# Kernel tuning notes

Hardware: AMD Instinct MI355X
Metric: run time of the kernel (lower is better)

The kernel has to match this reference:

```python
import jax, jax.numpy as jnp
import numpy as np

N_HEAD = 16

def setup_inputs() -> dict:
    key = jax.random.key(0)
    ks = jax.random.split(key, 9)
    B, T, C = 4, 2048, 1024
    s = 1.0 / np.sqrt(C)
    return {
        "x":  jax.random.normal(ks[0], (B, T, C), jnp.float32),
        "Wq": jax.random.normal(ks[1], (C, C), jnp.float32) * s,
        "bq": jax.random.normal(ks[2], (C,), jnp.float32) * 0.02,
        "Wk": jax.random.normal(ks[3], (C, C), jnp.float32) * s,
        "bk": jax.random.normal(ks[4], (C,), jnp.float32) * 0.02,
        "Wv": jax.random.normal(ks[5], (C, C), jnp.float32) * s,
        "bv": jax.random.normal(ks[6], (C,), jnp.float32) * 0.02,
        "Wp": jax.random.normal(ks[7], (C, C), jnp.float32) * s,
        "bp": jax.random.normal(ks[8], (C,), jnp.float32) * 0.02,
    }

def reference(x, Wq, bq, Wk, bk, Wv, bv, Wp, bp):
    B, T, C = x.shape
    H, D = N_HEAD, C // N_HEAD
    # torch nn.Linear: y = x @ W^T + b
    q = (x @ Wq.T + bq).reshape(B, T, H, D).transpose(0, 2, 1, 3)  # [B,H,T,D]
    k = (x @ Wk.T + bk).reshape(B, T, H, D).transpose(0, 2, 1, 3)
    v = (x @ Wv.T + bv).reshape(B, T, H, D).transpose(0, 2, 1, 3)
    # full TxT causal attention (non-flash path)
    att = jnp.einsum('bhtd,bhsd->bhts', q, k) * (1.0 / np.sqrt(D))  # [B,H,T,T]
    causal = jnp.tril(jnp.ones((T, T), dtype=bool))
    att = jnp.where(causal[None, None], att, -jnp.inf)
    att = jax.nn.softmax(att, axis=-1)
    y = jnp.einsum('bhts,bhsd->bhtd', att, v)  # [B,H,T,D]
    y = y.transpose(0, 2, 1, 3).reshape(B, T, C)
    return y @ Wp.T + bp
```

## Files before the change

### kernel.cpp

```cpp
#include <hip/hip_runtime.h>

typedef __bf16 bf16_t;
typedef __bf16 bf16x8 __attribute__((ext_vector_type(8)));
typedef float f32x4 __attribute__((ext_vector_type(4)));
typedef unsigned short ushort_t;

#define T_SEQ 2048
#define C_DIM 1024
#define NH    16
#define HD    64

__device__ __forceinline__ ushort_t f2bf(float f) {
    unsigned u = __builtin_bit_cast(unsigned, f);
    u += 0x7FFFu + ((u >> 16) & 1u);
    return (ushort_t)(u >> 16);
}

#define X4  2097152
#define W4  262144
__global__ __launch_bounds__(256)
void cvt_all_kernel(const float* __restrict__ x,  const float* __restrict__ Wq,
                    const float* __restrict__ Wk, const float* __restrict__ Wv,
                    ushort_t* __restrict__ xb,  ushort_t* __restrict__ Wqb,
                    ushort_t* __restrict__ Wkb, ushort_t* __restrict__ Wvb) {
    int i = blockIdx.x * 256 + threadIdx.x;
    const float* src; ushort_t* dst; int off;
    if (i < X4)                { src = x;  dst = xb;  off = i; }
    else if (i < X4 + W4)      { src = Wq; dst = Wqb; off = i - X4; }
    else if (i < X4 + 2 * W4)  { src = Wk; dst = Wkb; off = i - X4 - W4; }
    else                       { src = Wv; dst = Wvb; off = i - X4 - 2 * W4; }
    float4 f = ((const float4*)src)[off];
    ushort4 u;
    u.x = f2bf(f.x); u.y = f2bf(f.y); u.z = f2bf(f.z); u.w = f2bf(f.w);
    ((ushort4*)dst)[off] = u;
}

template<bool AF32, bool BF32>
__device__ __forceinline__ void gemm_core_128(const void* __restrict__ Araw,
                                              const void* __restrict__ Braw,
                                              f32x4 (&acc)[4][4]) {
    __shared__ alignas(16) ushort_t As[128 * 72];
    __shared__ alignas(16) ushort_t Ws[128 * 72];
    const int tid  = threadIdx.x;
    const int lane = tid & 63;
    const int wv   = tid >> 6;
    const int wm   = wv >> 1, wn = wv & 1;
    const int quad = lane >> 4, ln = lane & 15;
    const int m0 = blockIdx.x * 128, n0 = blockIdx.y * 128;

    f32x4 z4 = {0.f, 0.f, 0.f, 0.f};
#pragma unroll
    for (int i = 0; i < 4; i++)
#pragma unroll
        for (int j = 0; j < 4; j++) acc[i][j] = z4;

    for (int kt = 0; kt < 1024; kt += 64) {
        if (AF32) {
            const float* A = (const float*)Araw;
#pragma unroll
            for (int p = 0; p < 8; ++p) {
                int cid = p * 256 + tid;
                int row = cid >> 4, c4 = (cid & 15) * 4;
                float4 f = *(const float4*)(A + (size_t)(m0 + row) * 1024 + kt + c4);
                ushort4 u;
                u.x = f2bf(f.x); u.y = f2bf(f.y); u.z = f2bf(f.z); u.w = f2bf(f.w);
                *(ushort4*)&As[row * 72 + c4] = u;
            }
        } else {
            const bf16_t* A = (const bf16_t*)Araw;
#pragma unroll
            for (int p = 0; p < 4; ++p) {
                int cid = p * 256 + tid;
                int row = cid >> 3, c8 = (cid & 7) * 8;
                *(uint4*)&As[row * 72 + c8] =
                    *(const uint4*)(A + (size_t)(m0 + row) * 1024 + kt + c8);
            }
        }
        if (BF32) {
            const float* Bm = (const float*)Braw;
#pragma unroll
            for (int p = 0; p < 8; ++p) {
                int cid = p * 256 + tid;
                int row = cid >> 4, c4 = (cid & 15) * 4;
                float4 f = *(const float4*)(Bm + (size_t)(n0 + row) * 1024 + kt + c4);
                ushort4 u;
                u.x = f2bf(f.x); u.y = f2bf(f.y); u.z = f2bf(f.z); u.w = f2bf(f.w);
                *(ushort4*)&Ws[row * 72 + c4] = u;
            }
        } else {
            const bf16_t* Bm = (const bf16_t*)Braw;
#pragma unroll
            for (int p = 0; p < 4; ++p) {
                int cid = p * 256 + tid;
                int row = cid >> 3, c8 = (cid & 7) * 8;
                *(uint4*)&Ws[row * 72 + c8] =
                    *(const uint4*)(Bm + (size_t)(n0 + row) * 1024 + kt + c8);
            }
        }
        __syncthreads();
#pragma unroll
        for (int ks = 0; ks < 2; ++ks) {
            bf16x8 af[4], bfr[4];
#pragma unroll
            for (int i = 0; i < 4; i++)
                af[i] = *(const bf16x8*)&As[(wm * 64 + i * 16 + ln) * 72 + ks * 32 + quad * 8];
#pragma unroll
            for (int j = 0; j < 4; j++)
                bfr[j] = *(const bf16x8*)&Ws[(wn * 64 + j * 16 + ln) * 72 + ks * 32 + quad * 8];
#pragma unroll
            for (int i = 0; i < 4; i++)
#pragma unroll
                for (int j = 0; j < 4; j++)
                    acc[i][j] = __builtin_amdgcn_mfma_f32_16x16x32_bf16(af[i], bfr[j],
                                                                        acc[i][j], 0, 0, 0);
        }
        __syncthreads();
    }
}

__global__ __launch_bounds__(256, 2)
void qkv_gemm_kernel(const bf16_t* __restrict__ xb,
                     const bf16_t* __restrict__ Wqb, const float* __restrict__ bq,
                     const bf16_t* __restrict__ Wkb, const float* __restrict__ bk,
                     const bf16_t* __restrict__ Wvb, const float* __restrict__ bv,
                     ushort_t* __restrict__ Qo, ushort_t* __restrict__ Ko,
                     ushort_t* __restrict__ Vo) {
    const int z = blockIdx.z;
    const bf16_t* W   = (z == 0) ? Wqb : (z == 1) ? Wkb : Wvb;
    const float* bias = (z == 0) ? bq : (z == 1) ? bk : bv;
    ushort_t* outp    = (z == 0) ? Qo : (z == 1) ? Ko : Vo;
    const float fs    = (z == 0) ? 0.18033688011112042f : 1.0f;

    f32x4 acc[4][4];
    gemm_core_128<false, false>(xb, W, acc);

    const int tid  = threadIdx.x;
    const int lane = tid & 63;
    const int wv2  = tid >> 6;
    const int wm   = wv2 >> 1, wn = wv2 & 1;
    const int quad = lane >> 4, ln = lane & 15;
    const int mbase = blockIdx.x * 128 + wm * 64;
    const int nbase = blockIdx.y * 128 + wn * 64;

#pragma unroll
    for (int j = 0; j < 4; j++) {
        int n = nbase + j * 16 + ln;
        float bj = bias[n];
        int h = n >> 6, d = n & 63;
#pragma unroll
        for (int i = 0; i < 4; i++) {
            int mr = mbase + i * 16 + quad * 4;
            int b = mr >> 11;
            int t = mr & 2047;
            if (z < 2) {
                ushort_t* op = outp + ((size_t)(b * NH + h) * T_SEQ + t) * HD + d;
#pragma unroll
                for (int r = 0; r < 4; r++)
                    op[(size_t)r * HD] = f2bf((acc[i][j][r] + bj) * fs);
            } else {
                ushort4 us;
                us.x = f2bf(acc[i][j][0] + bj);
                us.y = f2bf(acc[i][j][1] + bj);
                us.z = f2bf(acc[i][j][2] + bj);
                us.w = f2bf(acc[i][j][3] + bj);
                *(ushort4*)(outp + ((size_t)(b * NH + h) * HD + d) * T_SEQ + t) = us;
            }
        }
    }
}

__device__ __forceinline__ void attn_tile(const ushort_t* __restrict__ Ks,
                                          const ushort_t* __restrict__ Vts,
                                          bf16_t* __restrict__ PsW,
                                          bf16x8 aq0, bf16x8 aq1, bf16x8 ones,
                                          f32x4 (&o)[4], f32x4& l4,
                                          bool diag, int wv, int quad, int ln) {
    f32x4 s4[4];
#pragma unroll
    for (int n16 = 0; n16 < 4; n16++) {
        f32x4 zz = {0.f, 0.f, 0.f, 0.f};
        bf16x8 bk0 = *(const bf16x8*)&Ks[(n16 * 16 + ln) * 72 + quad * 8];
        zz = __builtin_amdgcn_mfma_f32_16x16x32_bf16(aq0, bk0, zz, 0, 0, 0);
        bf16x8 bk1 = *(const bf16x8*)&Ks[(n16 * 16 + ln) * 72 + 32 + quad * 8];
        zz = __builtin_amdgcn_mfma_f32_16x16x32_bf16(aq1, bk1, zz, 0, 0, 0);
        s4[n16] = zz;
    }

#pragma unroll
    for (int n16 = 0; n16 < 4; n16++) {
#pragma unroll
        for (int r = 0; r < 4; r++) {
            float v = s4[n16][r];
            if (diag) {
                int sg = n16 * 16 + ln;
                int qg = wv * 16 + quad * 4 + r;
                if (sg > qg) v = -1e30f;
            }
            PsW[(quad * 4 + r) * 72 + n16 * 16 + ln] = (bf16_t)exp2f(v);
        }
    }

#pragma unroll
    for (int ks = 0; ks < 2; ks++) {
        bf16x8 ap = *(const bf16x8*)&PsW[ln * 72 + ks * 32 + quad * 8];
        l4 = __builtin_amdgcn_mfma_f32_16x16x32_bf16(ap, ones, l4, 0, 0, 0);
#pragma unroll
        for (int d16 = 0; d16 < 4; d16++) {
            bf16x8 bv = *(const bf16x8*)&Vts[(d16 * 16 + ln) * 72 + ks * 32 + quad * 8];
            o[d16] = __builtin_amdgcn_mfma_f32_16x16x32_bf16(ap, bv, o[d16], 0, 0, 0);
        }
    }
}

__global__ __launch_bounds__(256, 4)
void flash_kernel(const ushort_t* __restrict__ Qw, const ushort_t* __restrict__ Kw,
                  const ushort_t* __restrict__ Vt, ushort_t* __restrict__ Y) {
    __shared__ alignas(16) ushort_t Ks[64 * 72];
    __shared__ alignas(16) ushort_t Vts[64 * 72];
    __shared__ alignas(16) bf16_t PsA[4 * 16 * 72];
    __shared__ alignas(16) bf16_t PsB[4 * 16 * 72];

    const int tid  = threadIdx.x;
    const int lane = tid & 63;
    const int wv   = tid >> 6;
    const int quad = lane >> 4, ln = lane & 15;
    const int p  = blockIdx.x;
    const int bh = blockIdx.y;
    const int qa = p, qb = 31 - p;
    const int b = bh >> 4, h = bh & 15;
    bf16_t* PsWA = &PsA[wv * 1152];
    bf16_t* PsWB = &PsB[wv * 1152];

    bf16x8 ones;
#pragma unroll
    for (int i = 0; i < 8; i++) ones[i] = (bf16_t)1.0f;

    const ushort_t* qpa = Qw + ((size_t)bh * T_SEQ + qa * 64 + wv * 16 + ln) * HD;
    const ushort_t* qpb = Qw + ((size_t)bh * T_SEQ + qb * 64 + wv * 16 + ln) * HD;
    bf16x8 aqA0 = *(const bf16x8*)(qpa + quad * 8);
    bf16x8 aqA1 = *(const bf16x8*)(qpa + 32 + quad * 8);
    bf16x8 aqB0 = *(const bf16x8*)(qpb + quad * 8);
    bf16x8 aqB1 = *(const bf16x8*)(qpb + 32 + quad * 8);

    f32x4 oA[4], oB[4];
    f32x4 z4 = {0.f, 0.f, 0.f, 0.f};
#pragma unroll
    for (int i = 0; i < 4; i++) { oA[i] = z4; oB[i] = z4; }
    f32x4 lA4 = z4, lB4 = z4;

    const int row0 = tid >> 3, c80 = (tid & 7) * 8;
    const int row1 = (256 + tid) >> 3, c81 = c80;

    uint4 pk0, pk1, pv0, pv1;
    pk0 = *(const uint4*)(Kw + ((size_t)bh * T_SEQ + row0) * HD + c80);
    pv0 = *(const uint4*)(Vt + ((size_t)bh * HD + row0) * T_SEQ + c80);
    pk1 = *(const uint4*)(Kw + ((size_t)bh * T_SEQ + row1) * HD + c81);
    pv1 = *(const uint4*)(Vt + ((size_t)bh * HD + row1) * T_SEQ + c81);

    for (int st = 0; st <= qb; ++st) {
        __syncthreads();
        *(uint4*)&Ks[row0 * 72 + c80]  = pk0;
        *(uint4*)&Vts[row0 * 72 + c80] = pv0;
        *(uint4*)&Ks[row1 * 72 + c81]  = pk1;
        *(uint4*)&Vts[row1 * 72 + c81] = pv1;
        if (st < qb) {
            int s1 = (st + 1) * 64;
            pk0 = *(const uint4*)(Kw + ((size_t)bh * T_SEQ + s1 + row0) * HD + c80);
            pv0 = *(const uint4*)(Vt + ((size_t)bh * HD + row0) * T_SEQ + s1 + c80);
            pk1 = *(const uint4*)(Kw + ((size_t)bh * T_SEQ + s1 + row1) * HD + c81);
            pv1 = *(const uint4*)(Vt + ((size_t)bh * HD + row1) * T_SEQ + s1 + c81);
        }
        __syncthreads();

        if (st <= qa)
            attn_tile(Ks, Vts, PsWA, aqA0, aqA1, ones, oA, lA4, st == qa, wv, quad, ln);
        attn_tile(Ks, Vts, PsWB, aqB0, aqB1, ones, oB, lB4, st == qb, wv, quad, ln);
    }

#pragma unroll
    for (int ph = 0; ph < 2; ph++) {
        f32x4* o = ph ? oB : oA;
        f32x4 l4 = ph ? lB4 : lA4;
        int qt = ph ? qb : qa;
        f32x4 inv = {1.f / l4[0], 1.f / l4[1], 1.f / l4[2], 1.f / l4[3]};
        const int tg = qt * 64 + wv * 16 + quad * 4;
#pragma unroll
        for (int d16 = 0; d16 < 4; d16++) {
#pragma unroll
            for (int r = 0; r < 4; r++) {
                float v = o[d16][r] * inv[r];
                Y[((size_t)b * T_SEQ + tg + r) * C_DIM + h * HD + d16 * 16 + ln] = f2bf(v);
            }
        }
    }
}

__global__ __launch_bounds__(256, 2)
void proj_gemm_kernel(const bf16_t* __restrict__ Yw, const float* __restrict__ Wp,
                      const float* __restrict__ bp, float* __restrict__ out) {
    f32x4 acc[4][4];
    gemm_core_128<false, true>(Yw, Wp, acc);

    const int tid  = threadIdx.x;
    const int lane = tid & 63;
    const int wv2  = tid >> 6;
    const int wm   = wv2 >> 1, wn = wv2 & 1;
    const int quad = lane >> 4, ln = lane & 15;
    const int mbase = blockIdx.x * 128 + wm * 64;
    const int nbase = blockIdx.y * 128 + wn * 64;

#pragma unroll
    for (int j = 0; j < 4; j++) {
        int n = nbase + j * 16 + ln;
        float bj = bp[n];
#pragma unroll
        for (int i = 0; i < 4; i++) {
            int mr = mbase + i * 16 + quad * 4;
#pragma unroll
            for (int r = 0; r < 4; r++)
                out[(size_t)(mr + r) * C_DIM + n] = acc[i][j][r] + bj;
        }
    }
}

extern "C" void kernel_launch(void* const* d_in, const int* in_sizes, int n_in,
                              void* d_out, int out_size, void* d_ws, size_t ws_size,
                              hipStream_t stream) {
    const float* x  = (const float*)d_in[0];
    const float* Wq = (const float*)d_in[1];
    const float* bq = (const float*)d_in[2];
    const float* Wk = (const float*)d_in[3];
    const float* bk = (const float*)d_in[4];
    const float* Wv = (const float*)d_in[5];
    const float* bv = (const float*)d_in[6];
    const float* Wp = (const float*)d_in[7];
    const float* bp = (const float*)d_in[8];
    float* out = (float*)d_out;

    char* ws = (char*)d_ws;
    const size_t MB = (size_t)1 << 20;
    ushort_t* Qw = (ushort_t*)(ws);
    ushort_t* Kw = (ushort_t*)(ws + 16 * MB);
    ushort_t* Vt = (ushort_t*)(ws + 32 * MB);
    ushort_t* Yw = (ushort_t*)(ws + 48 * MB);

    ushort_t* xb  = (ushort_t*)out;
    ushort_t* Wqb = (ushort_t*)((char*)out + 16 * MB);
    ushort_t* Wkb = (ushort_t*)((char*)out + 18 * MB);
    ushort_t* Wvb = (ushort_t*)((char*)out + 20 * MB);

    cvt_all_kernel<<<11264, 256, 0, stream>>>(x, Wq, Wk, Wv, xb, Wqb, Wkb, Wvb);

    dim3 g1(64, 8, 3);
    qkv_gemm_kernel<<<g1, 256, 0, stream>>>((const bf16_t*)xb,
                                            (const bf16_t*)Wqb, bq,
                                            (const bf16_t*)Wkb, bk,
                                            (const bf16_t*)Wvb, bv,
                                            Qw, Kw, Vt);

    dim3 g2(16, 64);
    flash_kernel<<<g2, 256, 0, stream>>>(Qw, Kw, Vt, Yw);

    dim3 g3(64, 8, 1);
    proj_gemm_kernel<<<g3, 256, 0, stream>>>((const bf16_t*)Yw, Wp, bp, out);
}
```

Baseline: 274.2 us.

## Transpose QK MFMA for vectorized P stores, share V loads, remap block order

The QK^T MFMA operands are swapped so each lane holds four consecutive key columns. This lets the exp'd probabilities be packed into a single 4-wide bf16 LDS store instead of scalar scattered stores, and it uses the raw hardware exp2. The PV stage for both query tiles is merged into one loop, so each V fragment read from LDS feeds both tiles' MFMAs. Block indices are also remapped so concurrently scheduled blocks group heads with the same pair index, which may improve L2 reuse and balance. The merged loop adds register pressure and conditional MFMA paths.

```diff
diff --git a/kernel.cpp b/kernel.cpp
--- a/kernel.cpp
+++ b/kernel.cpp
@@ -2,6 +2,7 @@
 
 typedef __bf16 bf16_t;
 typedef __bf16 bf16x8 __attribute__((ext_vector_type(8)));
+typedef __bf16 bf16x4 __attribute__((ext_vector_type(4)));
 typedef float f32x4 __attribute__((ext_vector_type(4)));
 typedef unsigned short ushort_t;
 
@@ -169,46 +170,25 @@
     }
 }
 
-__device__ __forceinline__ void attn_tile(const ushort_t* __restrict__ Ks,
-                                          const ushort_t* __restrict__ Vts,
-                                          bf16_t* __restrict__ PsW,
-                                          bf16x8 aq0, bf16x8 aq1, bf16x8 ones,
-                                          f32x4 (&o)[4], f32x4& l4,
-                                          bool diag, int wv, int quad, int ln) {
-    f32x4 s4[4];
+__device__ __forceinline__ void qk_softmax(const ushort_t* __restrict__ Ks,
+                                           bf16_t* __restrict__ PsW,
+                                           bf16x8 aq0, bf16x8 aq1,
+                                           bool diag, int wv, int quad, int ln) {
 #pragma unroll
     for (int n16 = 0; n16 < 4; n16++) {
         f32x4 zz = {0.f, 0.f, 0.f, 0.f};
         bf16x8 bk0 = *(const bf16x8*)&Ks[(n16 * 16 + ln) * 72 + quad * 8];
-        zz = __builtin_amdgcn_mfma_f32_16x16x32_bf16(aq0, bk0, zz, 0, 0, 0);
+        zz = __builtin_amdgcn_mfma_f32_16x16x32_bf16(bk0, aq0, zz, 0, 0, 0);
         bf16x8 bk1 = *(const bf16x8*)&Ks[(n16 * 16 + ln) * 72 + 32 + quad * 8];
-        zz = __builtin_amdgcn_mfma_f32_16x16x32_bf16(aq1, bk1, zz, 0, 0, 0);
-        s4[n16] = zz;
-    }
-
-#pragma unroll
-    for (int n16 = 0; n16 < 4; n16++) {
+        zz = __builtin_amdgcn_mfma_f32_16x16x32_bf16(bk1, aq1, zz, 0, 0, 0);
+        bf16x4 pb;
 #pragma unroll
         for (int r = 0; r < 4; r++) {
-            float v = s4[n16][r];
-            if (diag) {
-                int sg = n16 * 16 + ln;
-                int qg = wv * 16 + quad * 4 + r;
-                if (sg > qg) v = -1e30f;
-            }
-            PsW[(quad * 4 + r) * 72 + n16 * 16 + ln] = (bf16_t)exp2f(v);
-        }
-    }
-
-#pragma unroll
-    for (int ks = 0; ks < 2; ks++) {
-        bf16x8 ap = *(const bf16x8*)&PsW[ln * 72 + ks * 32 + quad * 8];
-        l4 = __builtin_amdgcn_mfma_f32_16x16x32_bf16(ap, ones, l4, 0, 0, 0);
-#pragma unroll
-        for (int d16 = 0; d16 < 4; d16++) {
-            bf16x8 bv = *(const bf16x8*)&Vts[(d16 * 16 + ln) * 72 + ks * 32 + quad * 8];
-            o[d16] = __builtin_amdgcn_mfma_f32_16x16x32_bf16(ap, bv, o[d16], 0, 0, 0);
-        }
+            float v = zz[r];
+            v = (diag && (n16 * 16 + quad * 4 + r > wv * 16 + ln)) ? -1e30f : v;
+            pb[r] = (bf16_t)__builtin_amdgcn_exp2f(v);
+        }
+        *(bf16x4*)&PsW[ln * 72 + n16 * 16 + quad * 4] = pb;
     }
 }
 
@@ -224,8 +204,10 @@
     const int lane = tid & 63;
     const int wv   = tid >> 6;
     const int quad = lane >> 4, ln = lane & 15;
-    const int p  = blockIdx.x;
-    const int bh = blockIdx.y;
+    const int L  = blockIdx.y * 16 + blockIdx.x;
+    const int m  = L >> 3;
+    const int bh = ((m >> 4) << 3) | (L & 7);
+    const int p  = m & 15;
     const int qa = p, qb = 31 - p;
     const int b = bh >> 4, h = bh & 15;
     bf16_t* PsWA = &PsA[wv * 1152];
@@ -272,9 +254,28 @@
         }
         __syncthreads();
 
-        if (st <= qa)
-            attn_tile(Ks, Vts, PsWA, aqA0, aqA1, ones, oA, lA4, st == qa, wv, quad, ln);
-        attn_tile(Ks, Vts, PsWB, aqB0, aqB1, ones, oB, lB4, st == qb, wv, quad, ln);
+        const bool doA = (st <= qa);
+        if (doA)
+            qk_softmax(Ks, PsWA, aqA0, aqA1, st == qa, wv, quad, ln);
+        qk_softmax(Ks, PsWB, aqB0, aqB1, st == qb, wv, quad, ln);
+
+#pragma unroll
+        for (int ks = 0; ks < 2; ks++) {
+            bf16x8 apA, apB;
+            if (doA) {
+                apA = *(const bf16x8*)&PsWA[ln * 72 + ks * 32 + quad * 8];
+                lA4 = __builtin_amdgcn_mfma_f32_16x16x32_bf16(apA, ones, lA4, 0, 0, 0);
+            }
+            apB = *(const bf16x8*)&PsWB[ln * 72 + ks * 32 + quad * 8];
+            lB4 = __builtin_amdgcn_mfma_f32_16x16x32_bf16(apB, ones, lB4, 0, 0, 0);
+#pragma unroll
+            for (int d16 = 0; d16 < 4; d16++) {
+                bf16x8 bv = *(const bf16x8*)&Vts[(d16 * 16 + ln) * 72 + ks * 32 + quad * 8];
+                if (doA)
+                    oA[d16] = __builtin_amdgcn_mfma_f32_16x16x32_bf16(apA, bv, oA[d16], 0, 0, 0);
+                oB[d16] = __builtin_amdgcn_mfma_f32_16x16x32_bf16(apB, bv, oB[d16], 0, 0, 0);
+            }
+        }
     }
 
 #pragma unroll
```

Measured after the change: 265.3 us. 3.2% less time.
